# Kernel tuning notes

Measured on AMD Instinct MI355X. Metric: run time of the kernel, lower is better.

Reference implementation:

```python
import jax, jax.numpy as jnp
import numpy as np

B, S, D, H = 4, 1024, 1024, 16
E = D // H  # head_dim = 64
N = 2 * H  # number of slots


def _ln(x, g, b, eps=1e-5):
    m = x.mean(-1, keepdims=True)
    v = ((x - m) ** 2).mean(-1, keepdims=True)
    return (x - m) / jnp.sqrt(v + eps) * g + b


def _feat(x):
    # F.elu(x, 1.0) + 1.0
    return jax.nn.elu(x) + 1.0


def setup_inputs() -> dict:
    key = jax.random.key(0)
    ks = jax.random.split(key, 40)
    w = lambda k, shape: jax.random.normal(k, shape, jnp.float32) * 0.02
    z = lambda shape: jnp.zeros(shape, jnp.float32)
    o = lambda shape: jnp.ones(shape, jnp.float32)
    return {
        'x': jax.random.normal(ks[0], (B, S, D), jnp.float32),
        'ln1_g': o(D), 'ln1_b': z(D), 'ln2_g': o(D), 'ln2_b': z(D),
        'Wq': w(ks[1], (D, D)), 'bq': z(D),
        'Wk': w(ks[2], (D, D)), 'bk': z(D),
        'Wv': w(ks[3], (D, D)), 'bv': z(D),
        'Wf': w(ks[4], (D, D)), 'bf': z(D),
        'Wr1': w(ks[5], (D, 2 * D)), 'br1': z(2 * D),
        'Wr2': w(ks[6], (2 * D, D)), 'br2': z(D),
        'Wip': w(ks[7], (D, N * E)), 'bip': z(N * E),
        'Wtq': w(ks[8], (E, E)), 'btq': z(E),
        'Wtk': w(ks[9], (E, E)), 'btk': z(E),
        'Wtv': w(ks[10], (E, E)), 'btv': z(E),
        'lnp_g': o(E), 'lnp_b': z(E),
        'Wl1': w(ks[11], (E, 2 * E)), 'bl1': z(2 * E),
        'Wl2': w(ks[12], (2 * E, E)), 'bl2': z(E),
        'Wsp': w(ks[13], (2 * E, E)), 'bsp': z(E),
    }


def reference(x, ln1_g, ln1_b, ln2_g, ln2_b, Wq, bq, Wk, bk, Wv, bv, Wf, bf,
              Wr1, br1, Wr2, br2, Wip, bip, Wtq, btq, Wtk, btk, Wtv, btv,
              lnp_g, lnp_b, Wl1, bl1, Wl2, bl2, Wsp, bsp):
    xn = _ln(x, ln1_g, ln1_b)
    # main q/k/v
    q = (xn @ Wq + bq).reshape(B, S, H, E).transpose(0, 2, 1, 3) / np.sqrt(E)  # [B,H,S,E]
    k = (xn @ Wk + bk).reshape(B, S, H, E)
    v = (xn @ Wv + bv).reshape(B, S, H, E)
    kv0 = jnp.concatenate([k, v], axis=2)  # [B,S,2H,E] initial slots

    # --- competitive (slot) attention, 3 iterations ---
    inp = (xn @ Wip + bip).reshape(B, S, N, E)
    kk = _feat(inp @ Wtk + btk)          # [B,S,N,E]
    vv = inp @ Wtv + btv                 # [B,S,N,E]
    slots = kv0
    scale = 1.0 / E                      # slot_size = head_dim
    for _ in range(3):
        qq = (slots @ Wtq + btq) + kv0
        qq = _feat(qq * (E ** -0.5))
        logits = jnp.einsum('bswe,bsne->bswn', kk, qq)
        attn = jax.nn.softmax(logits, axis=3) + 1e-6
        attn = attn / attn.sum(axis=2, keepdims=True)
        upd = jnp.einsum('bswn,bswe->bsne', attn, vv)
        h = _ln(upd, lnp_g, lnp_b)
        h = jax.nn.relu(h @ Wl1 + bl1) @ Wl2 + bl2
        slots = slots + h * scale
    # slot_dropout is eval-mode identity
    slots = jnp.concatenate([kv0, slots], axis=-1) @ Wsp + bsp  # [B,S,2H,E]

    k2 = slots[:, :, :H].transpose(0, 2, 3, 1)  # [B,H,E,S]
    v2 = slots[:, :, H:].transpose(0, 2, 1, 3)  # [B,H,S,E]
    qf = _feat(q)
    kf = _feat(k2)
    score = qf @ kf                              # [B,H,S,S]
    score = score / (score.sum(-1, keepdims=True) + 1e-5)
    out = (score @ v2).transpose(0, 2, 1, 3).reshape(B, S, D)
    out = out @ Wf + bf
    out = x + out
    res = out
    h = _ln(out, ln2_g, ln2_b)
    h = jax.nn.relu(h @ Wr1 + br1) @ Wr2 + br2  # dropouts are eval-mode identity
    return res + h
```

## Files before the change

### kernel.cpp

```cpp
#include <hip/hip_runtime.h>
#include <hip/hip_bf16.h>

typedef __hip_bfloat16 bf16t;
typedef short short8 __attribute__((ext_vector_type(8)));
typedef float f32x4 __attribute__((ext_vector_type(4)));


__device__ __forceinline__ float featf(float x) { return x > 0.f ? x + 1.f : __expf(x); }
__device__ __forceinline__ float featf_s(float x) { return x > 0.f ? x + 1.f : expf(x); }
__device__ __forceinline__ float frcp(float x) { return __builtin_amdgcn_rcpf(x); }
__device__ __forceinline__ float ldf(const bf16t* p, size_t i) { return __bfloat162float(p[i]); }
__device__ __forceinline__ float ldf(const float* p, size_t i) { return p[i]; }
__device__ __forceinline__ void stf(bf16t* p, size_t i, float v) { p[i] = __float2bfloat16(v); }
__device__ __forceinline__ void stf(float* p, size_t i, float v) { p[i] = v; }
__device__ __forceinline__ float b2f(unsigned short u) {
    unsigned int x = ((unsigned int)u) << 16; float f; __builtin_memcpy(&f, &x, 4); return f;
}
__device__ __forceinline__ unsigned short f2b(float f) {
    bf16t h = __float2bfloat16(f); unsigned short u; __builtin_memcpy(&u, &h, 2); return u;
}
__device__ __forceinline__ void gl_lds16(const short* g, short* l) {
    __builtin_amdgcn_global_load_lds((const __attribute__((address_space(1))) unsigned int*)g,
                                     (__attribute__((address_space(3))) unsigned int*)l, 16, 0, 0);
}
#define MFMA16(a, b, c) __builtin_amdgcn_mfma_f32_16x16x32_bf16((a), (b), (c), 0, 0, 0)

__global__ __launch_bounds__(256) void fill_k(float* __restrict__ out, int n, float v) {
    int i = blockIdx.x * 256 + threadIdx.x;
    if (i < n) out[i] = v;
}

__global__ __launch_bounds__(256) void multi_transpose_k(const float* __restrict__ s0, const float* __restrict__ s1,
                                                         const float* __restrict__ s2, const float* __restrict__ s3,
                                                         bf16t* __restrict__ d0, bf16t* __restrict__ d1,
                                                         bf16t* __restrict__ d2, bf16t* __restrict__ d3,
                                                         int R0, int C0, int R1, int C1, int R2, int C2, int R3, int C3,
                                                         int e0, int e1, int e2) {
    __shared__ bf16t tile[32][33];
    int b = blockIdx.x;
    const float* W; bf16t* Wt; int C, R, lb;
    if (b < e0)      { W = s0; Wt = d0; R = R0; C = C0; lb = b; }
    else if (b < e1) { W = s1; Wt = d1; R = R1; C = C1; lb = b - e0; }
    else if (b < e2) { W = s2; Wt = d2; R = R2; C = C2; lb = b - e1; }
    else             { W = s3; Wt = d3; R = R3; C = C3; lb = b - e2; }
    int tiles_c = C >> 5;
    int c0 = (lb % tiles_c) * 32, r0 = (lb / tiles_c) * 32;
    int tx = threadIdx.x & 31, ty = threadIdx.x >> 5;
    #pragma unroll
    for (int i = 0; i < 32; i += 8)
        tile[ty + i][tx] = __float2bfloat16(W[(size_t)(r0 + ty + i) * C + (c0 + tx)]);
    __syncthreads();
    #pragma unroll
    for (int i = 0; i < 32; i += 8)
        Wt[(size_t)(c0 + ty + i) * R + (r0 + tx)] = tile[tx][ty + i];
}

__global__ __launch_bounds__(256) void small_prep_k(const float* __restrict__ Wtk,
                                                    const float* __restrict__ Wtv,
                                                    const float* __restrict__ Wtq,
                                                    const float* __restrict__ Wl1,
                                                    const float* __restrict__ Wl2,
                                                    const float* __restrict__ Wsp,
                                                    const float* __restrict__ bk,
                                                    const float* __restrict__ bv,
                                                    const float* __restrict__ bip,
                                                    const float* __restrict__ bq,
                                                    const float* __restrict__ btk,
                                                    const float* __restrict__ btv,
                                                    bf16t* __restrict__ WtkvT,
                                                    bf16t* __restrict__ WtqI,
                                                    bf16t* __restrict__ Wl1T,
                                                    bf16t* __restrict__ Wl2T,
                                                    bf16t* __restrict__ WspT,
                                                    float* __restrict__ bcat,
                                                    float* __restrict__ bcat2) {
    int b = blockIdx.x, tid = threadIdx.x;
    if (b == 0) {
        for (int i = tid; i < 8192; i += 256) {
            int n2 = i >> 6, e = i & 63;
            float v = (n2 < 64) ? Wtk[e * 64 + n2] : Wtv[e * 64 + (n2 - 64)];
            WtkvT[i] = __float2bfloat16(v);
        }
    } else if (b == 1) {
        for (int i = tid; i < 8192; i += 256) {
            int e = i >> 7, k = i & 127;
            float v = (k < 64) ? Wtq[k * 64 + e] : ((k - 64 == e) ? 1.f : 0.f);
            WtqI[i] = __float2bfloat16(v);
        }
    } else if (b == 2) {
        for (int i = tid; i < 8192; i += 256) { int n = i >> 6, k = i & 63; Wl1T[i] = __float2bfloat16(Wl1[k * 128 + n]); }
    } else if (b == 3) {
        for (int i = tid; i < 8192; i += 256) { int n = i >> 7, k = i & 127; Wl2T[i] = __float2bfloat16(Wl2[k * 64 + n]); }
    } else if (b == 4) {
        for (int i = tid; i < 8192; i += 256) { int n = i >> 7, k = i & 127; WspT[i] = __float2bfloat16(Wsp[k * 64 + n]); }
    } else if (b == 5) {
        for (int i = tid; i < 5120; i += 256) {
            float v;
            if (i < 1024) v = bk[i];
            else if (i < 2048) v = bv[i - 1024];
            else if (i < 4096) v = bip[i - 2048];
            else v = bq[i - 4096];
            bcat[i] = v;
        }
    } else {
        if (tid < 128) bcat2[tid] = (tid < 64) ? btk[tid] : btv[tid - 64];
    }
}

__global__ __launch_bounds__(256) void ln_kernel(const float* __restrict__ X,
                                                 const float* __restrict__ g,
                                                 const float* __restrict__ b,
                                                 bf16t* __restrict__ Y) {
    int t = blockIdx.x, tid = threadIdx.x;
    size_t base = (size_t)t * 1024 + tid * 4;
    float v0 = X[base + 0], v1 = X[base + 1], v2 = X[base + 2], v3 = X[base + 3];
    float s = v0 + v1 + v2 + v3;
    float q = v0 * v0 + v1 * v1 + v2 * v2 + v3 * v3;
    __shared__ float rs[4], rq[4];
    for (int o = 32; o > 0; o >>= 1) { s += __shfl_down(s, o); q += __shfl_down(q, o); }
    int wid = tid >> 6, lane = tid & 63;
    if (lane == 0) { rs[wid] = s; rq[wid] = q; }
    __syncthreads();
    float S = rs[0] + rs[1] + rs[2] + rs[3];
    float Q = rq[0] + rq[1] + rq[2] + rq[3];
    float mean = S * (1.f / 1024.f);
    float var = Q * (1.f / 1024.f) - mean * mean;
    float rstd = rsqrtf(var + 1e-5f);
    int c = tid * 4;
    stf(Y, base + 0, (v0 - mean) * rstd * g[c + 0] + b[c + 0]);
    stf(Y, base + 1, (v1 - mean) * rstd * g[c + 1] + b[c + 1]);
    stf(Y, base + 2, (v2 - mean) * rstd * g[c + 2] + b[c + 2]);
    stf(Y, base + 3, (v3 - mean) * rstd * g[c + 3] + b[c + 3]);
}

template <int MODE, typename TC, typename TADD>
__global__ __launch_bounds__(256) void gemm128_k(const bf16t* __restrict__ A,
                                                 const bf16t* __restrict__ Bt,
                                                 const float* __restrict__ bias,
                                                 const TADD* __restrict__ add,
                                                 TC* __restrict__ C,
                                                 int M, int N, int K, int ldC) {
    __shared__ short As[128 * 32];
    __shared__ short Bs[128 * 32];
    int tid = threadIdx.x;
    int wave = tid >> 6, lane = tid & 63;
    int l16 = lane & 15, quad = lane >> 4;
    int tilesM = M >> 7;
    int tm = blockIdx.x % tilesM;
    int tn = blockIdx.x / tilesM;
    int wm = wave >> 1, wn = wave & 1;

    int lrow = lane >> 2;
    int lseg = (lane & 3) * 8;
    const short* Ag = (const short*)A + (size_t)(tm * 128 + wave * 32 + lrow) * K + lseg;
    const short* Ag2 = Ag + (size_t)16 * K;
    const short* Bg = (const short*)Bt + (size_t)(tn * 128 + wave * 32 + lrow) * K + lseg;
    const short* Bg2 = Bg + (size_t)16 * K;
    short* Asw = As + (wave * 32) * 32;
    short* Asw2 = Asw + 16 * 32;
    short* Bsw = Bs + (wave * 32) * 32;
    short* Bsw2 = Bsw + 16 * 32;

    f32x4 acc[4][4] = {};
    for (int k0 = 0; k0 < K; k0 += 32) {
        gl_lds16(Ag + k0, Asw);
        gl_lds16(Ag2 + k0, Asw2);
        gl_lds16(Bg + k0, Bsw);
        gl_lds16(Bg2 + k0, Bsw2);
        __syncthreads();
        short8 av[4], bv[4];
        #pragma unroll
        for (int i = 0; i < 4; i++)
            av[i] = *(const short8*)(As + (wm * 64 + i * 16 + l16) * 32 + quad * 8);
        #pragma unroll
        for (int j = 0; j < 4; j++)
            bv[j] = *(const short8*)(Bs + (wn * 64 + j * 16 + l16) * 32 + quad * 8);
        #pragma unroll
        for (int i = 0; i < 4; i++)
            #pragma unroll
            for (int j = 0; j < 4; j++)
                acc[i][j] = MFMA16(av[i], bv[j], acc[i][j]);
        __syncthreads();
    }

    #pragma unroll
    for (int j = 0; j < 4; j++) {
        int col = tn * 128 + wn * 64 + j * 16 + l16;
        float bcol = bias[col];
        #pragma unroll
        for (int i = 0; i < 4; i++) {
            int row0 = tm * 128 + wm * 64 + i * 16 + quad * 4;
            #pragma unroll
            for (int r = 0; r < 4; r++) {
                int row = row0 + r;
                float v = acc[i][j][r] + bcol;
                float outv;
                if constexpr (MODE == 0) outv = v;
                else if constexpr (MODE == 4) outv = fmaxf(v, 0.f);
                else if constexpr (MODE == 5) outv = v + ldf(add, (size_t)row * N + col);
                else outv = v;
                stf(C, (size_t)row * ldC + col, outv);
            }
        }
    }
}

__global__ __launch_bounds__(256) void gemm_proj_k(const bf16t* __restrict__ A,
                                                   const bf16t* __restrict__ Bt,
                                                   const float* __restrict__ bias,
                                                   bf16t* __restrict__ kv0,
                                                   bf16t* __restrict__ inp,
                                                   bf16t* __restrict__ qf) {
    __shared__ short As[128 * 32];
    __shared__ short Bs[128 * 32];
    const int K = 1024;
    int tid = threadIdx.x;
    int wave = tid >> 6, lane = tid & 63;
    int l16 = lane & 15, quad = lane >> 4;
    int tm = blockIdx.x & 31;
    int tn = blockIdx.x >> 5;
    int wm = wave >> 1, wn = wave & 1;

    int lrow = lane >> 2;
    int lseg = (lane & 3) * 8;
    const short* Ag = (const short*)A + (size_t)(tm * 128 + wave * 32 + lrow) * K + lseg;
    const short* Ag2 = Ag + (size_t)16 * K;
    const short* Bg = (const short*)Bt + (size_t)(tn * 128 + wave * 32 + lrow) * K + lseg;
    const short* Bg2 = Bg + (size_t)16 * K;
    short* Asw = As + (wave * 32) * 32;
    short* Asw2 = Asw + 16 * 32;
    short* Bsw = Bs + (wave * 32) * 32;
    short* Bsw2 = Bsw + 16 * 32;

    f32x4 acc[4][4] = {};
    for (int k0 = 0; k0 < K; k0 += 32) {
        gl_lds16(Ag + k0, Asw);
        gl_lds16(Ag2 + k0, Asw2);
        gl_lds16(Bg + k0, Bsw);
        gl_lds16(Bg2 + k0, Bsw2);
        __syncthreads();
        short8 av[4], bv[4];
        #pragma unroll
        for (int i = 0; i < 4; i++)
            av[i] = *(const short8*)(As + (wm * 64 + i * 16 + l16) * 32 + quad * 8);
        #pragma unroll
        for (int j = 0; j < 4; j++)
            bv[j] = *(const short8*)(Bs + (wn * 64 + j * 16 + l16) * 32 + quad * 8);
        #pragma unroll
        for (int i = 0; i < 4; i++)
            #pragma unroll
            for (int j = 0; j < 4; j++)
                acc[i][j] = MFMA16(av[i], bv[j], acc[i][j]);
        __syncthreads();
    }

    #pragma unroll
    for (int j = 0; j < 4; j++) {
        int col = tn * 128 + wn * 64 + j * 16 + l16;
        float bcol = bias[col];
        #pragma unroll
        for (int i = 0; i < 4; i++) {
            int row0 = tm * 128 + wm * 64 + i * 16 + quad * 4;
            #pragma unroll
            for (int r = 0; r < 4; r++) {
                int row = row0 + r;
                float v = acc[i][j][r] + bcol;
                if (tn < 16) stf(kv0, (size_t)row * 2048 + col, v);
                else if (tn < 32) stf(inp, (size_t)row * 2048 + (col - 2048), v);
                else stf(qf, (size_t)row * 1024 + (col - 4096), featf(v * 0.125f));
            }
        }
    }
}

__global__ __launch_bounds__(256) void gemm_kv_k(const bf16t* __restrict__ A,
                                                 const bf16t* __restrict__ Bt,
                                                 const float* __restrict__ bias,
                                                 bf16t* __restrict__ kkO,
                                                 bf16t* __restrict__ vvTO) {
    int wave = threadIdx.x >> 6, lane = threadIdx.x & 63;
    int tile = blockIdx.x * 4 + wave;
    int tm = tile >> 1, tn = tile & 1;
    int l16 = lane & 15, quad = lane >> 4;
    f32x4 acc[4][4] = {};
    const short* Ab = (const short*)A + (size_t)(tm * 64 + l16) * 64;
    const short* Bb = (const short*)Bt + (size_t)(tn * 64 + l16) * 64;
    #pragma unroll
    for (int k0 = 0; k0 < 64; k0 += 32) {
        int ka = k0 + quad * 8;
        short8 av[4], bv[4];
        #pragma unroll
        for (int i = 0; i < 4; i++) av[i] = *(const short8*)(Ab + (size_t)i * 16 * 64 + ka);
        #pragma unroll
        for (int j = 0; j < 4; j++) bv[j] = *(const short8*)(Bb + (size_t)j * 16 * 64 + ka);
        #pragma unroll
        for (int i = 0; i < 4; i++)
            #pragma unroll
            for (int j = 0; j < 4; j++)
                acc[i][j] = MFMA16(av[i], bv[j], acc[i][j]);
    }
    #pragma unroll
    for (int j = 0; j < 4; j++) {
        int col = j * 16 + l16;
        float bcol = bias[tn * 64 + col];
        #pragma unroll
        for (int i = 0; i < 4; i++) {
            int row0 = tm * 64 + i * 16 + quad * 4;
            #pragma unroll
            for (int r = 0; r < 4; r++) {
                int row = row0 + r;
                float v = acc[i][j][r] + bcol;
                if (tn == 0) kkO[(size_t)row * 64 + col] = __float2bfloat16(featf(v));
                else stf(vvTO, (size_t)(row >> 5) * 2048 + (size_t)col * 32 + (row & 31), v);
            }
        }
    }
}

__global__ __launch_bounds__(256) void gemm_cat_k(const bf16t* __restrict__ A1,
                                                  const bf16t* __restrict__ A2,
                                                  const bf16t* __restrict__ Bt,
                                                  const float* __restrict__ bias,
                                                  bf16t* __restrict__ C, int M) {
    int wave = threadIdx.x >> 6;
    int lane = threadIdx.x & 63;
    int tiles = M >> 6;
    int tile = blockIdx.x * 4 + wave;
    if (tile >= tiles) return;
    int tm = tile;
    int l16 = lane & 15, quad = lane >> 4;
    f32x4 acc[4][4] = {};
    #pragma unroll
    for (int p = 0; p < 2; p++) {
        const short* Ab = (const short*)(p ? A2 : A1) + (size_t)(tm * 64 + l16) * 64;
        const short* Bb = (const short*)Bt + (size_t)l16 * 128 + p * 64;
        #pragma unroll
        for (int k0 = 0; k0 < 64; k0 += 32) {
            int ka = k0 + quad * 8;
            short8 av[4], bv[4];
            #pragma unroll
            for (int i = 0; i < 4; i++) av[i] = *(const short8*)(Ab + (size_t)i * 16 * 64 + ka);
            #pragma unroll
            for (int j = 0; j < 4; j++) bv[j] = *(const short8*)(Bb + (size_t)j * 16 * 128 + ka);
            #pragma unroll
            for (int i = 0; i < 4; i++)
                #pragma unroll
                for (int j = 0; j < 4; j++)
                    acc[i][j] = MFMA16(av[i], bv[j], acc[i][j]);
        }
    }
    #pragma unroll
    for (int j = 0; j < 4; j++) {
        int col = j * 16 + l16;
        float bcol = bias[col];
        #pragma unroll
        for (int i = 0; i < 4; i++) {
            int row0 = tm * 64 + i * 16 + quad * 4;
            #pragma unroll
            for (int r = 0; r < 4; r++)
                C[(size_t)(row0 + r) * 64 + col] = __float2bfloat16(acc[i][j][r] + bcol);
        }
    }
}

__global__ __launch_bounds__(256) void slot_all_k(const bf16t* __restrict__ kv0,
                                                  const bf16t* __restrict__ kk,
                                                  const bf16t* __restrict__ vvT,
                                                  const bf16t* __restrict__ WtqI,
                                                  const float* __restrict__ btq,
                                                  const float* __restrict__ lnpg,
                                                  const float* __restrict__ lnpb,
                                                  const bf16t* __restrict__ Wl1T,
                                                  const float* __restrict__ bl1,
                                                  const bf16t* __restrict__ Wl2T,
                                                  const float* __restrict__ bl2,
                                                  bf16t* __restrict__ slots_out,
                                                  int zoff) {
    __shared__ short slotsS[4][32 * 72];
    __shared__ short scratch[4][32 * 72];
    int wave = threadIdx.x >> 6, lane = threadIdx.x & 63;
    int l16 = lane & 15, quad = lane >> 4;
    int t = blockIdx.x * 4 + wave;
    short* S = slotsS[wave];
    short* X = scratch[wave];
    size_t tbase = (size_t)t * 2048;

    {
        const short* src = (const short*)kv0 + tbase;
        #pragma unroll
        for (int p = 0; p < 4; p++) {
            int idx = p * 512 + lane * 8;
            int row = idx >> 6, col = idx & 63;
            *(short8*)(S + row * 72 + col) = *(const short8*)(src + idx);
        }
    }

    #pragma unroll 1
    for (int it = 0; it < 3; it++) {
        int vo = it * zoff;
        f32x4 aq[2][4] = {};
        #pragma unroll
        for (int k0 = 0; k0 < 4; k0++) {
            short8 af[2];
            #pragma unroll
            for (int i = 0; i < 2; i++) {
                if (k0 < 2)
                    af[i] = *(const short8*)(S + (i * 16 + l16) * 72 + k0 * 32 + quad * 8);
                else
                    af[i] = *(const short8*)((const short*)kv0 + tbase + (size_t)((i * 16 + l16) * 64 + (k0 - 2) * 32 + quad * 8 + vo));
            }
            #pragma unroll
            for (int j = 0; j < 4; j++) {
                short8 bf_ = *(const short8*)((const short*)WtqI + (size_t)((j * 16 + l16) * 128 + k0 * 32 + quad * 8 + vo));
                #pragma unroll
                for (int i = 0; i < 2; i++) aq[i][j] = MFMA16(af[i], bf_, aq[i][j]);
            }
        }
        {
            float btqv[4];
            #pragma unroll
            for (int j = 0; j < 4; j++) btqv[j] = btq[j * 16 + l16 + vo];
            #pragma unroll
            for (int i = 0; i < 2; i++)
                #pragma unroll
                for (int j = 0; j < 4; j++)
                    #pragma unroll
                    for (int r = 0; r < 4; r++) {
                        int n = i * 16 + quad * 4 + r, e = j * 16 + l16;
                        X[n * 72 + e] = (short)f2b(featf_s((aq[i][j][r] + btqv[j]) * 0.125f));
                    }
        }
        f32x4 al[2][2] = {};
        #pragma unroll
        for (int k0 = 0; k0 < 2; k0++) {
            short8 ak[2], bf_[2];
            #pragma unroll
            for (int i = 0; i < 2; i++)
                ak[i] = *(const short8*)((const short*)kk + tbase + (size_t)((i * 16 + l16) * 64 + k0 * 32 + quad * 8 + vo));
            #pragma unroll
            for (int j = 0; j < 2; j++)
                bf_[j] = *(const short8*)(X + (j * 16 + l16) * 72 + k0 * 32 + quad * 8);
            #pragma unroll
            for (int i = 0; i < 2; i++)
                #pragma unroll
                for (int j = 0; j < 2; j++)
                    al[i][j] = MFMA16(ak[i], bf_[j], al[i][j]);
        }
        #pragma unroll
        for (int i = 0; i < 2; i++)
            #pragma unroll
            for (int r = 0; r < 4; r++) {
                float m = fmaxf(al[i][0][r], al[i][1][r]);
                #pragma unroll
                for (int d = 1; d < 16; d <<= 1) m = fmaxf(m, __shfl_xor(m, d));
                float e0 = expf(al[i][0][r] - m), e1 = expf(al[i][1][r] - m);
                float s = e0 + e1;
                #pragma unroll
                for (int d = 1; d < 16; d <<= 1) s += __shfl_xor(s, d);
                float inv = 1.f / s;
                al[i][0][r] = e0 * inv + 1e-6f;
                al[i][1][r] = e1 * inv + 1e-6f;
            }
        #pragma unroll
        for (int j = 0; j < 2; j++) {
            float cs = 0.f;
            #pragma unroll
            for (int i = 0; i < 2; i++)
                #pragma unroll
                for (int r = 0; r < 4; r++) cs += al[i][j][r];
            cs += __shfl_xor(cs, 16);
            cs += __shfl_xor(cs, 32);
            float inv = 1.f / cs;
            #pragma unroll
            for (int i = 0; i < 2; i++)
                #pragma unroll
                for (int r = 0; r < 4; r++) al[i][j][r] *= inv;
        }
        #pragma unroll
        for (int i = 0; i < 2; i++)
            #pragma unroll
            for (int j = 0; j < 2; j++)
                #pragma unroll
                for (int r = 0; r < 4; r++) {
                    int w = i * 16 + quad * 4 + r, n = j * 16 + l16;
                    X[n * 40 + w] = (short)f2b(al[i][j][r]);
                }
        f32x4 au[2][4] = {};
        {
            short8 af[2];
            #pragma unroll
            for (int i = 0; i < 2; i++)
                af[i] = *(const short8*)(X + (i * 16 + l16) * 40 + quad * 8);
            #pragma unroll
            for (int j = 0; j < 4; j++) {
                short8 bf_ = *(const short8*)((const short*)vvT + tbase + (size_t)((j * 16 + l16) * 32 + quad * 8 + vo));
                #pragma unroll
                for (int i = 0; i < 2; i++) au[i][j] = MFMA16(af[i], bf_, au[i][j]);
            }
        }
        {
            float lgv[4], lbv[4];
            #pragma unroll
            for (int j = 0; j < 4; j++) { lgv[j] = lnpg[j * 16 + l16 + vo]; lbv[j] = lnpb[j * 16 + l16 + vo]; }
            #pragma unroll
            for (int i = 0; i < 2; i++)
                #pragma unroll
                for (int r = 0; r < 4; r++) {
                    float s1 = 0.f, s2 = 0.f;
                    #pragma unroll
                    for (int j = 0; j < 4; j++) { float u = au[i][j][r]; s1 += u; s2 += u * u; }
                    #pragma unroll
                    for (int d = 1; d < 16; d <<= 1) { s1 += __shfl_xor(s1, d); s2 += __shfl_xor(s2, d); }
                    float mean = s1 * (1.f / 64.f);
                    float var = s2 * (1.f / 64.f) - mean * mean;
                    float rstd = rsqrtf(var + 1e-5f);
                    int n = i * 16 + quad * 4 + r;
                    #pragma unroll
                    for (int j = 0; j < 4; j++)
                        X[n * 72 + j * 16 + l16] = (short)f2b((au[i][j][r] - mean) * rstd * lgv[j] + lbv[j]);
                }
        }
        short8 a1[2][2];
        #pragma unroll
        for (int i = 0; i < 2; i++)
            #pragma unroll
            for (int k0 = 0; k0 < 2; k0++)
                a1[i][k0] = *(const short8*)(X + (i * 16 + l16) * 72 + k0 * 32 + quad * 8);
        f32x4 ac2[2][4] = {};
        #pragma unroll
        for (int c = 0; c < 2; c++) {
            f32x4 ac1[2][4] = {};
            #pragma unroll
            for (int k0 = 0; k0 < 2; k0++)
                #pragma unroll
                for (int j = 0; j < 4; j++) {
                    short8 bf_ = *(const short8*)((const short*)Wl1T + (size_t)(((c * 4 + j) * 16 + l16) * 64 + k0 * 32 + quad * 8 + vo));
                    #pragma unroll
                    for (int i = 0; i < 2; i++) ac1[i][j] = MFMA16(a1[i][k0], bf_, ac1[i][j]);
                }
            {
                float bl1v[4];
                #pragma unroll
                for (int j = 0; j < 4; j++) bl1v[j] = bl1[(c * 4 + j) * 16 + l16 + vo];
                #pragma unroll
                for (int i = 0; i < 2; i++)
                    #pragma unroll
                    for (int j = 0; j < 4; j++)
                        #pragma unroll
                        for (int r = 0; r < 4; r++) {
                            int n = i * 16 + quad * 4 + r;
                            X[n * 72 + j * 16 + l16] = (short)f2b(fmaxf(ac1[i][j][r] + bl1v[j], 0.f));
                        }
            }
            #pragma unroll
            for (int kc = 0; kc < 2; kc++) {
                short8 a2[2];
                #pragma unroll
                for (int i = 0; i < 2; i++)
                    a2[i] = *(const short8*)(X + (i * 16 + l16) * 72 + kc * 32 + quad * 8);
                int k1 = c * 2 + kc;
                #pragma unroll
                for (int j = 0; j < 4; j++) {
                    short8 bf_ = *(const short8*)((const short*)Wl2T + (size_t)((j * 16 + l16) * 128 + k1 * 32 + quad * 8 + vo));
                    #pragma unroll
                    for (int i = 0; i < 2; i++) ac2[i][j] = MFMA16(a2[i], bf_, ac2[i][j]);
                }
            }
        }
        {
            float bl2v[4];
            #pragma unroll
            for (int j = 0; j < 4; j++) bl2v[j] = bl2[j * 16 + l16 + vo];
            #pragma unroll
            for (int i = 0; i < 2; i++)
                #pragma unroll
                for (int j = 0; j < 4; j++)
                    #pragma unroll
                    for (int r = 0; r < 4; r++) {
                        int n = i * 16 + quad * 4 + r, e = j * 16 + l16;
                        float old = b2f((unsigned short)S[n * 72 + e]);
                        S[n * 72 + e] = (short)f2b(old + (ac2[i][j][r] + bl2v[j]) * (1.f / 64.f));
                    }
        }
    }
    {
        short* dst = (short*)slots_out + tbase;
        #pragma unroll
        for (int p = 0; p < 4; p++) {
            int idx = p * 512 + lane * 8;
            int row = idx >> 6, col = idx & 63;
            *(short8*)(dst + idx) = *(const short8*)(S + row * 72 + col);
        }
    }
}

__global__ __launch_bounds__(256) void kv_outer_k(const bf16t* __restrict__ slotsO,
                                                  float* __restrict__ Kpart,
                                                  float* __restrict__ kspart) {
    __shared__ short kfT[64 * 72];
    __shared__ short v2T[64 * 72];
    __shared__ float ksred[8][64];
    int blk = blockIdx.x;
    int bh = blk >> 2, chunk = blk & 3;
    int b = bh >> 4, h = bh & 15;
    int tid = threadIdx.x;
    int wave = tid >> 6, lane = tid & 63;
    int l16 = lane & 15, quad = lane >> 4;
    int m0 = wave * 16;

    int sgrp = tid >> 5;
    int e0 = (tid & 31) * 2;
    float ks0 = 0.f, ks1 = 0.f;
    f32x4 acc[4];
    #pragma unroll
    for (int j = 0; j < 4; j++) acc[j] = (f32x4){0.f, 0.f, 0.f, 0.f};

    for (int tile = chunk * 4; tile < chunk * 4 + 4; tile++) {
        #pragma unroll
        for (int p = 0; p < 8; p++) {
            int sl = p * 8 + sgrp;
            size_t row = ((size_t)(b * 1024 + tile * 64 + sl)) * 2048;
            unsigned int dk = *(const unsigned int*)((const unsigned short*)slotsO + row + h * 64 + e0);
            float f0 = featf(b2f((unsigned short)(dk & 0xffff)));
            float f1 = featf(b2f((unsigned short)(dk >> 16)));
            ks0 += f0; ks1 += f1;
            kfT[e0 * 72 + sl] = (short)f2b(f0);
            kfT[(e0 + 1) * 72 + sl] = (short)f2b(f1);
            unsigned int dv = *(const unsigned int*)((const unsigned short*)slotsO + row + (16 + h) * 64 + e0);
            v2T[e0 * 72 + sl] = (short)(dv & 0xffff);
            v2T[(e0 + 1) * 72 + sl] = (short)(dv >> 16);
        }
        __syncthreads();
        #pragma unroll
        for (int k2 = 0; k2 < 2; k2++) {
            short8 a = *(const short8*)(kfT + (m0 + l16) * 72 + k2 * 32 + quad * 8);
            #pragma unroll
            for (int j = 0; j < 4; j++) {
                short8 bv = *(const short8*)(v2T + (j * 16 + l16) * 72 + k2 * 32 + quad * 8);
                acc[j] = MFMA16(a, bv, acc[j]);
            }
        }
        __syncthreads();
    }

    float* Km = Kpart + (size_t)blk * 4096;
    #pragma unroll
    for (int j = 0; j < 4; j++)
        #pragma unroll
        for (int r = 0; r < 4; r++)
            Km[(m0 + quad * 4 + r) * 64 + j * 16 + l16] = acc[j][r];

    ksred[sgrp][e0] = ks0;
    ksred[sgrp][e0 + 1] = ks1;
    __syncthreads();
    if (tid < 64) {
        float s = 0.f;
        #pragma unroll
        for (int r = 0; r < 8; r++) s += ksred[r][tid];
        kspart[blk * 64 + tid] = s;
    }
}

__global__ __launch_bounds__(256) void kred_k(const float* __restrict__ Kpart,
                                              const float* __restrict__ kspart,
                                              float* __restrict__ Kmat,
                                              float* __restrict__ ksum) {
    int gid = blockIdx.x * 256 + threadIdx.x;
    int idx = gid * 4;
    int bh = idx >> 12, j = idx & 4095;
    const float* p = Kpart + (size_t)(bh * 4) * 4096 + j;
    f32x4 a = *(const f32x4*)p;
    f32x4 bq = *(const f32x4*)(p + 4096);
    f32x4 c = *(const f32x4*)(p + 8192);
    f32x4 d = *(const f32x4*)(p + 12288);
    f32x4 r = a + bq + c + d;
    *(f32x4*)(Kmat + idx) = r;
    if (gid < 4096) {
        int bh2 = gid >> 6, e = gid & 63;
        const float* q = kspart + (size_t)(bh2 * 4) * 64 + e;
        ksum[gid] = q[0] + q[64] + q[128] + q[192];
    }
}

__global__ __launch_bounds__(256) void attn_out_k(const bf16t* __restrict__ qf,
                                                  const float* __restrict__ Kmat,
                                                  const float* __restrict__ ksum,
                                                  bf16t* __restrict__ out) {
    int t = blockIdx.x, tid = threadIdx.x;
    int b = t >> 10;
    __shared__ float q[16 * 65];
    __shared__ float dinv[16];
    for (int i = tid; i < 1024; i += 256) {
        int h = i >> 6, e = i & 63;
        q[h * 65 + e] = __bfloat162float(qf[(size_t)t * 1024 + i]);
    }
    __syncthreads();
    {
        int h = tid >> 4, e0 = (tid & 15) * 4;
        const float* ks = ksum + (size_t)(b * 16 + h) * 64 + e0;
        const float* qh = q + h * 65 + e0;
        float d = qh[0] * ks[0] + qh[1] * ks[1] + qh[2] * ks[2] + qh[3] * ks[3];
        #pragma unroll
        for (int dlt = 1; dlt < 16; dlt <<= 1) d += __shfl_xor(d, dlt);
        if ((tid & 15) == 0) dinv[h] = frcp(d + 1e-5f);
    }
    __syncthreads();
    int h = tid >> 4, j0 = (tid & 15) * 4;
    const float* Km = Kmat + (size_t)(b * 16 + h) * 4096;
    float a0 = 0.f, a1 = 0.f, a2 = 0.f, a3 = 0.f;
    for (int e = 0; e < 64; e++) {
        float qe = q[h * 65 + e];
        const float* kr = Km + e * 64 + j0;
        a0 += qe * kr[0]; a1 += qe * kr[1]; a2 += qe * kr[2]; a3 += qe * kr[3];
    }
    float di = dinv[h];
    size_t ob = (size_t)t * 1024 + h * 64 + j0;
    out[ob + 0] = __float2bfloat16(a0 * di);
    out[ob + 1] = __float2bfloat16(a1 * di);
    out[ob + 2] = __float2bfloat16(a2 * di);
    out[ob + 3] = __float2bfloat16(a3 * di);
}

#define LAUNCH_GEMM128(MODE, TCT, TADDT, A_, Bt_, bias_, add_, C_, M_, N_, K_, ldC_)         \
    do {                                                                                     \
        int tiles__ = ((M_) >> 7) * ((N_) >> 7);                                             \
        gemm128_k<MODE, TCT, TADDT><<<tiles__, 256, 0, stream>>>(                            \
            (const bf16t*)(A_), (const bf16t*)(Bt_), (const float*)(bias_),                  \
            (const TADDT*)(add_), (TCT*)(C_), (M_), (N_), (K_), (ldC_));                     \
    } while (0)

extern "C" void kernel_launch(void* const* d_in, const int* in_sizes, int n_in,
                              void* d_out, int out_size, void* d_ws, size_t ws_size,
                              hipStream_t stream) {
    (void)in_sizes; (void)n_in;
    const float* x    = (const float*)d_in[0];
    const float* ln1g = (const float*)d_in[1];
    const float* ln1b = (const float*)d_in[2];
    const float* ln2g = (const float*)d_in[3];
    const float* ln2b = (const float*)d_in[4];
    const float* Wq  = (const float*)d_in[5];  const float* bq  = (const float*)d_in[6];
    const float* Wk  = (const float*)d_in[7];  const float* bk  = (const float*)d_in[8];
    const float* Wv  = (const float*)d_in[9];  const float* bv  = (const float*)d_in[10];
    const float* Wf  = (const float*)d_in[11]; const float* bWf = (const float*)d_in[12];
    const float* Wr1 = (const float*)d_in[13]; const float* br1 = (const float*)d_in[14];
    const float* Wr2 = (const float*)d_in[15]; const float* br2 = (const float*)d_in[16];
    const float* Wip = (const float*)d_in[17]; const float* bip = (const float*)d_in[18];
    const float* Wtq = (const float*)d_in[19]; const float* btq = (const float*)d_in[20];
    const float* Wtk = (const float*)d_in[21]; const float* btk = (const float*)d_in[22];
    const float* Wtv = (const float*)d_in[23]; const float* btv = (const float*)d_in[24];
    const float* lnpg= (const float*)d_in[25]; const float* lnpb= (const float*)d_in[26];
    const float* Wl1 = (const float*)d_in[27]; const float* bl1 = (const float*)d_in[28];
    const float* Wl2 = (const float*)d_in[29]; const float* bl2 = (const float*)d_in[30];
    const float* Wsp = (const float*)d_in[31]; const float* bsp = (const float*)d_in[32];

    char* ws = (char*)d_ws;
    size_t off = 0;
    auto alloc = [&](size_t bytes) -> char* {
        off = (off + 255) & ~(size_t)255;
        char* p = ws + off;
        off += bytes;
        return p;
    };
    const size_t T = 4096, TS = 131072;
    const size_t MB8 = T * 1024 * 2, MB16 = T * 2048 * 2;
    bf16t* R_xn   = (bf16t*)alloc(MB8);
    bf16t* R_h1   = (bf16t*)alloc(MB8);
    bf16t* R_kv0  = (bf16t*)alloc(MB16);
    bf16t* R_inp  = (bf16t*)alloc(MB16);
    bf16t* R_kk   = (bf16t*)alloc(MB16);
    bf16t* R_vv   = (bf16t*)alloc(MB16);
    bf16t* R_sl   = (bf16t*)alloc(MB16);
    bf16t* Wcat   = (bf16t*)alloc(5120 * 1024 * 2);
    bf16t* WtkvT = (bf16t*)alloc(128 * 64 * 2);
    bf16t* WtqI = (bf16t*)alloc(64 * 128 * 2);
    bf16t* Wl1T = (bf16t*)alloc(128 * 64 * 2);
    bf16t* Wl2T = (bf16t*)alloc(64 * 128 * 2);
    bf16t* WspT = (bf16t*)alloc(64 * 128 * 2);
    float* bcat = (float*)alloc(5120 * 4);
    float* bcat2 = (float*)alloc(128 * 4);
    float* Kmat = (float*)alloc(64 * 4096 * 4);
    float* ksum = (float*)alloc(64 * 64 * 4);
    float* Kpart = (float*)alloc(256 * 4096 * 4);
    float* kspart = (float*)alloc(256 * 64 * 4);

    if (off > ws_size) {
        fill_k<<<(out_size + 255) / 256, 256, 0, stream>>>((float*)d_out, out_size, 1000.f);
        return;
    }
    float* R_res = (float*)R_vv;
    bf16t* WfT  = R_kv0;
    bf16t* Wr1T = R_kv0 + (size_t)1024 * 1024;
    bf16t* Wr2T = R_kv0 + (size_t)3072 * 1024;

    small_prep_k<<<7, 256, 0, stream>>>(Wtk, Wtv, Wtq, Wl1, Wl2, Wsp, bk, bv, bip, bq, btk, btv,
                                        WtkvT, WtqI, Wl1T, Wl2T, WspT, bcat, bcat2);

    ln_kernel<<<4096, 256, 0, stream>>>(x, ln1g, ln1b, R_xn);

    multi_transpose_k<<<5120, 256, 0, stream>>>(
        Wk, Wv, Wip, Wq,
        Wcat, Wcat + (size_t)1024 * 1024, Wcat + (size_t)2048 * 1024, Wcat + (size_t)4096 * 1024,
        1024, 1024, 1024, 1024, 1024, 2048, 1024, 1024,
        1024, 2048, 4096);

    gemm_proj_k<<<1280, 256, 0, stream>>>(R_xn, Wcat, bcat, R_kv0, R_inp, R_h1);

    gemm_kv_k<<<1024, 256, 0, stream>>>(R_inp, WtkvT, bcat2, R_kk, R_vv);

    slot_all_k<<<1024, 256, 0, stream>>>(R_kv0, R_kk, R_vv, WtqI, btq, lnpg, lnpb,
                                         Wl1T, bl1, Wl2T, bl2, R_sl, 0);

    gemm_cat_k<<<512, 256, 0, stream>>>(R_kv0, R_sl, WspT, bsp, R_kk, 131072);

    multi_transpose_k<<<5120, 256, 0, stream>>>(
        Wf, Wr1, Wr2, Wr2,
        WfT, Wr1T, Wr2T, Wr2T,
        1024, 1024, 1024, 2048, 2048, 1024, 2048, 1024,
        1024, 3072, 5120);

    kv_outer_k<<<256, 256, 0, stream>>>(R_kk, Kpart, kspart);
    kred_k<<<256, 256, 0, stream>>>(Kpart, kspart, Kmat, ksum);

    attn_out_k<<<4096, 256, 0, stream>>>(R_h1, Kmat, ksum, R_inp);

    LAUNCH_GEMM128(5, float, float, R_inp, WfT, bWf, x, R_res, 4096, 1024, 1024, 1024);

    ln_kernel<<<4096, 256, 0, stream>>>(R_res, ln2g, ln2b, R_xn);
    LAUNCH_GEMM128(4, bf16t, bf16t, R_xn, Wr1T, br1, nullptr, R_sl, 4096, 2048, 1024, 2048);
    LAUNCH_GEMM128(5, float, float, R_sl, Wr2T, br2, R_res, (float*)d_out, 4096, 1024, 2048, 1024);
}
```

Before: 543.5 us.

## Compute linear-attention output with MFMA and swizzle GEMM block order

The per-token scalar attn_out kernel is replaced by two kernels. One computes the per-token, per-head denominators. The other multiplies qf by a bf16 transposed K-V matrix using MFMA tiles. kv_outer now produces the transposed product so kred can store it as bf16, which cuts its size and loses some precision. The GEMM kernels also remap block indices across groups of 8, likely to spread tiles across XCDs for better L2 locality.

```diff
diff --git a/kernel.cpp b/kernel.cpp
--- a/kernel.cpp
+++ b/kernel.cpp
@@ -3,6 +3,7 @@
 
 typedef __hip_bfloat16 bf16t;
 typedef short short8 __attribute__((ext_vector_type(8)));
+typedef short short4v __attribute__((ext_vector_type(4)));
 typedef float f32x4 __attribute__((ext_vector_type(4)));
 
 
@@ -146,8 +147,9 @@
     int wave = tid >> 6, lane = tid & 63;
     int l16 = lane & 15, quad = lane >> 4;
     int tilesM = M >> 7;
-    int tm = blockIdx.x % tilesM;
-    int tn = blockIdx.x / tilesM;
+    int bid = (blockIdx.x & 7) * (gridDim.x >> 3) + (blockIdx.x >> 3);
+    int tm = bid % tilesM;
+    int tn = bid / tilesM;
     int wm = wave >> 1, wn = wave & 1;
 
     int lrow = lane >> 2;
@@ -217,8 +219,9 @@
     int tid = threadIdx.x;
     int wave = tid >> 6, lane = tid & 63;
     int l16 = lane & 15, quad = lane >> 4;
-    int tm = blockIdx.x & 31;
-    int tn = blockIdx.x >> 5;
+    int bid = (blockIdx.x & 7) * (gridDim.x >> 3) + (blockIdx.x >> 3);
+    int tm = bid & 31;
+    int tn = bid >> 5;
     int wm = wave >> 1, wn = wave & 1;
 
     int lrow = lane >> 2;
@@ -633,10 +636,10 @@
         __syncthreads();
         #pragma unroll
         for (int k2 = 0; k2 < 2; k2++) {
-            short8 a = *(const short8*)(kfT + (m0 + l16) * 72 + k2 * 32 + quad * 8);
+            short8 a = *(const short8*)(v2T + (m0 + l16) * 72 + k2 * 32 + quad * 8);
             #pragma unroll
             for (int j = 0; j < 4; j++) {
-                short8 bv = *(const short8*)(v2T + (j * 16 + l16) * 72 + k2 * 32 + quad * 8);
+                short8 bv = *(const short8*)(kfT + (j * 16 + l16) * 72 + k2 * 32 + quad * 8);
                 acc[j] = MFMA16(a, bv, acc[j]);
             }
         }
@@ -663,7 +666,7 @@
 
 __global__ __launch_bounds__(256) void kred_k(const float* __restrict__ Kpart,
                                               const float* __restrict__ kspart,
-                                              float* __restrict__ Kmat,
+                                              bf16t* __restrict__ KmatT,
                                               float* __restrict__ ksum) {
     int gid = blockIdx.x * 256 + threadIdx.x;
     int idx = gid * 4;
@@ -674,7 +677,10 @@
     f32x4 c = *(const f32x4*)(p + 8192);
     f32x4 d = *(const f32x4*)(p + 12288);
     f32x4 r = a + bq + c + d;
-    *(f32x4*)(Kmat + idx) = r;
+    short4v o;
+    #pragma unroll
+    for (int k = 0; k < 4; k++) o[k] = (short)f2b(r[k]);
+    *(short4v*)((short*)KmatT + idx) = o;
     if (gid < 4096) {
         int bh2 = gid >> 6, e = gid & 63;
         const float* q = kspart + (size_t)(bh2 * 4) * 64 + e;
@@ -682,43 +688,60 @@
     }
 }
 
-__global__ __launch_bounds__(256) void attn_out_k(const bf16t* __restrict__ qf,
-                                                  const float* __restrict__ Kmat,
+__global__ __launch_bounds__(256) void attn_den_k(const bf16t* __restrict__ qf,
                                                   const float* __restrict__ ksum,
-                                                  bf16t* __restrict__ out) {
-    int t = blockIdx.x, tid = threadIdx.x;
-    int b = t >> 10;
-    __shared__ float q[16 * 65];
-    __shared__ float dinv[16];
-    for (int i = tid; i < 1024; i += 256) {
-        int h = i >> 6, e = i & 63;
-        q[h * 65 + e] = __bfloat162float(qf[(size_t)t * 1024 + i]);
-    }
-    __syncthreads();
-    {
-        int h = tid >> 4, e0 = (tid & 15) * 4;
-        const float* ks = ksum + (size_t)(b * 16 + h) * 64 + e0;
-        const float* qh = q + h * 65 + e0;
-        float d = qh[0] * ks[0] + qh[1] * ks[1] + qh[2] * ks[2] + qh[3] * ks[3];
-        #pragma unroll
-        for (int dlt = 1; dlt < 16; dlt <<= 1) d += __shfl_xor(d, dlt);
-        if ((tid & 15) == 0) dinv[h] = frcp(d + 1e-5f);
-    }
-    __syncthreads();
-    int h = tid >> 4, j0 = (tid & 15) * 4;
-    const float* Km = Kmat + (size_t)(b * 16 + h) * 4096;
-    float a0 = 0.f, a1 = 0.f, a2 = 0.f, a3 = 0.f;
-    for (int e = 0; e < 64; e++) {
-        float qe = q[h * 65 + e];
-        const float* kr = Km + e * 64 + j0;
-        a0 += qe * kr[0]; a1 += qe * kr[1]; a2 += qe * kr[2]; a3 += qe * kr[3];
-    }
-    float di = dinv[h];
-    size_t ob = (size_t)t * 1024 + h * 64 + j0;
-    out[ob + 0] = __float2bfloat16(a0 * di);
-    out[ob + 1] = __float2bfloat16(a1 * di);
-    out[ob + 2] = __float2bfloat16(a2 * di);
-    out[ob + 3] = __float2bfloat16(a3 * di);
+                                                  float* __restrict__ dinv) {
+    int t0 = blockIdx.x * 16;
+    int b = t0 >> 10;
+    int tok = threadIdx.x >> 4, h = threadIdx.x & 15;
+    int t = t0 + tok;
+    const unsigned short* qr = (const unsigned short*)qf + (size_t)t * 1024 + h * 64;
+    const float* ks = ksum + (size_t)(b * 16 + h) * 64;
+    float d = 0.f;
+    #pragma unroll
+    for (int e = 0; e < 64; e++) d += b2f(qr[e]) * ks[e];
+    dinv[t * 16 + h] = 1.f / (d + 1e-5f);
+}
+
+__global__ __launch_bounds__(256) void attn_gemm_k(const bf16t* __restrict__ qf,
+                                                   const bf16t* __restrict__ KmatT,
+                                                   const float* __restrict__ dinv,
+                                                   bf16t* __restrict__ out) {
+    int wave = threadIdx.x >> 6, lane = threadIdx.x & 63;
+    int wt = blockIdx.x * 4 + wave;
+    int bh = wt >> 4, st = wt & 15;
+    int b = bh >> 4, h = bh & 15;
+    int l16 = lane & 15, quad = lane >> 4;
+    int s0 = st * 64;
+    const short* Aq = (const short*)qf + (size_t)(b * 1024 + s0 + l16) * 1024 + h * 64;
+    const short* Bk = (const short*)KmatT + (size_t)bh * 4096;
+    f32x4 acc[4][4] = {};
+    #pragma unroll
+    for (int k0 = 0; k0 < 64; k0 += 32) {
+        int ka = k0 + quad * 8;
+        short8 av[4], bv[4];
+        #pragma unroll
+        for (int i = 0; i < 4; i++) av[i] = *(const short8*)(Aq + (size_t)i * 16 * 1024 + ka);
+        #pragma unroll
+        for (int j = 0; j < 4; j++) bv[j] = *(const short8*)(Bk + (j * 16 + l16) * 64 + ka);
+        #pragma unroll
+        for (int i = 0; i < 4; i++)
+            #pragma unroll
+            for (int j = 0; j < 4; j++)
+                acc[i][j] = MFMA16(av[i], bv[j], acc[i][j]);
+    }
+    #pragma unroll
+    for (int i = 0; i < 4; i++) {
+        #pragma unroll
+        for (int r = 0; r < 4; r++) {
+            int t = b * 1024 + s0 + i * 16 + quad * 4 + r;
+            float di = dinv[t * 16 + h];
+            size_t ob = (size_t)t * 1024 + h * 64;
+            #pragma unroll
+            for (int j = 0; j < 4; j++)
+                out[ob + j * 16 + l16] = __float2bfloat16(acc[i][j][r] * di);
+        }
+    }
 }
 
 #define LAUNCH_GEMM128(MODE, TCT, TADDT, A_, Bt_, bias_, add_, C_, M_, N_, K_, ldC_)         \
@@ -778,10 +801,11 @@
     bf16t* WspT = (bf16t*)alloc(64 * 128 * 2);
     float* bcat = (float*)alloc(5120 * 4);
     float* bcat2 = (float*)alloc(128 * 4);
-    float* Kmat = (float*)alloc(64 * 4096 * 4);
+    bf16t* KmatT = (bf16t*)alloc(64 * 4096 * 2);
     float* ksum = (float*)alloc(64 * 64 * 4);
     float* Kpart = (float*)alloc(256 * 4096 * 4);
     float* kspart = (float*)alloc(256 * 64 * 4);
+    float* dinv = (float*)alloc((size_t)4096 * 16 * 4);
 
     if (off > ws_size) {
         fill_k<<<(out_size + 255) / 256, 256, 0, stream>>>((float*)d_out, out_size, 1000.f);
@@ -819,9 +843,10 @@
         1024, 3072, 5120);
 
     kv_outer_k<<<256, 256, 0, stream>>>(R_kk, Kpart, kspart);
-    kred_k<<<256, 256, 0, stream>>>(Kpart, kspart, Kmat, ksum);
-
-    attn_out_k<<<4096, 256, 0, stream>>>(R_h1, Kmat, ksum, R_inp);
+    kred_k<<<256, 256, 0, stream>>>(Kpart, kspart, KmatT, ksum);
+    attn_den_k<<<256, 256, 0, stream>>>(R_h1, ksum, dinv);
+
+    attn_gemm_k<<<256, 256, 0, stream>>>(R_h1, KmatT, dinv, R_inp);
 
     LAUNCH_GEMM128(5, float, float, R_inp, WfT, bWf, x, R_res, 4096, 1024, 1024, 1024);
 
```

New measurement: 538.5 us. No clear change (-0.9%).
